# Kernel optimization log

Hardware: AMD Instinct MI355X
Metric: run time of the kernel (lower is better)

The kernel has to match this reference:

```python
import jax, jax.numpy as jnp
import numpy as np

P_X, P_Y = 2, 2  # pooling window (matches init_kwargs)


def setup_inputs() -> dict:
    key = jax.random.key(0)
    k1, k2 = jax.random.split(key)
    B, C, n, m = 32, 64, 128, 128
    s = jax.random.normal(k1, (B, C, n, m), dtype=jnp.float32)
    # multinomial weight vectors, one per (i, j, k) in loop order i->j->k
    etas = jax.random.uniform(k2, (n * m * C, P_X * P_Y), dtype=jnp.float32)
    return {"s": s, "etas": etas}


def reference(s, etas):
    B, C, n, m = s.shape
    P = P_X * P_Y
    # torch.multinomial(eta, 1) == categorical with logits log(eta)
    key = jax.random.key(42)
    logits = jnp.log(jnp.maximum(etas, 1e-30))
    zeta = jax.random.categorical(key, logits, axis=-1)          # [n*m*C]
    # cnt order is (i, j, k) -> reshape to [n, m, C], move C first
    onehot = jax.nn.one_hot(zeta, P, dtype=s.dtype)
    onehot = onehot.reshape(n, m, C, P).transpose(2, 0, 1, 3)     # [C, n, m, P]
    # scatter s value into the sampled slot of each p_x*p_y tile
    tiles = s[..., None] * onehot[None]                           # [B, C, n, m, P]
    tiles = tiles.reshape(B, C, n, m, P_X, P_Y)
    out = tiles.transpose(0, 1, 2, 4, 3, 5).reshape(B, C, n * P_X, m * P_Y)
    return out
```

## Files before the change

### kernel.cpp

```cpp
#include <hip/hip_runtime.h>
#include <math.h>
#include <stdint.h>


#define NROWS 1048576u

#define KS0 0u
#define KS1 42u
#define KS2 0x1BD11BF0u

__device__ __forceinline__ void threefry2x32(uint32_t x0, uint32_t x1,
                                             uint32_t& o0, uint32_t& o1) {
  x0 += KS0; x1 += KS1;
#define TF_RND(R) { x0 += x1; x1 = (x1 << (R)) | (x1 >> (32 - (R))); x1 ^= x0; }
  TF_RND(13) TF_RND(15) TF_RND(26) TF_RND(6)
  x0 += KS1; x1 += KS2 + 1u;
  TF_RND(17) TF_RND(29) TF_RND(16) TF_RND(24)
  x0 += KS2; x1 += KS0 + 2u;
  TF_RND(13) TF_RND(15) TF_RND(26) TF_RND(6)
  x0 += KS0; x1 += KS1 + 3u;
  TF_RND(17) TF_RND(29) TF_RND(16) TF_RND(24)
  x0 += KS1; x1 += KS2 + 4u;
  TF_RND(13) TF_RND(15) TF_RND(26) TF_RND(6)
  x0 += KS2; x1 += KS0 + 5u;
#undef TF_RND
  o0 = x0; o1 = x1;
}

__device__ __forceinline__ float bits_to_unit(uint32_t b) {
  float u = __uint_as_float((b >> 9) | 0x3F800000u) - 1.0f;
  return (u == 0.0f) ? 1.17549435e-38f : u;
}

__device__ __forceinline__ int argmax_gumbel(const float* u, const float* eta) {
  float best = -3.4e38f; int bi = 0;
  #pragma unroll
  for (int p = 0; p < 4; ++p) {
    float inner = (float)log((double)u[p]);
    float g     = -(float)log(-(double)inner);
    float logit = (float)log((double)fmaxf(eta[p], 1e-30f));
    float score = g + logit;
    if (score > best) { best = score; bi = p; }
  }
  return bi;
}

__global__ __launch_bounds__(256) void zeta_kernel(const float4* __restrict__ etas,
                                                   uint8_t* __restrict__ zc) {
  const uint32_t t = blockIdx.x * 256u + threadIdx.x;
  float u[4];
  #pragma unroll
  for (int p = 0; p < 4; ++p) {
    uint32_t o0, o1;
    threefry2x32(0u, 4u * t + (uint32_t)p, o0, o1);
    u[p] = bits_to_unit(o0 ^ o1);
  }
  const float4 e4 = etas[t];
  const float eta[4] = {e4.x, e4.y, e4.z, e4.w};
  const int z = argmax_gumbel(u, eta);
  zc[(t & 63u) * 16384u + (t >> 6)] = (uint8_t)z;
}

__global__ __launch_bounds__(256) void scatter_kernel(const float* __restrict__ s,
                                                      const uint8_t* __restrict__ zc,
                                                      float4* __restrict__ out) {
  const uint32_t t  = blockIdx.x * 256u + threadIdx.x;
  const uint32_t yq = t & 63u;
  const uint32_t x  = (t >> 6) & 255u;
  const uint32_t bc = t >> 14;
  const uint32_t c  = bc & 63u;
  const uint32_t i  = x >> 1, px = x & 1u;
  const uint32_t j0 = yq << 1;
  const float2 s2 = *reinterpret_cast<const float2*>(
      &s[((size_t)bc << 14) + (i << 7) + j0]);
  const uint32_t zidx = c * 16384u + (i << 7) + j0;
  const uint8_t z0 = zc[zidx], z1 = zc[zidx + 1u];
  const uint32_t p0 = px << 1, p1 = p0 + 1u;
  float4 o;
  o.x = (z0 == (uint8_t)p0) ? s2.x : 0.0f;
  o.y = (z0 == (uint8_t)p1) ? s2.x : 0.0f;
  o.z = (z1 == (uint8_t)p0) ? s2.y : 0.0f;
  o.w = (z1 == (uint8_t)p1) ? s2.y : 0.0f;
  out[t] = o;
}

extern "C" void kernel_launch(void* const* d_in, const int* in_sizes, int n_in,
                              void* d_out, int out_size, void* d_ws, size_t ws_size,
                              hipStream_t stream) {
  const float*  s    = (const float*)d_in[0];
  const float4* etas = (const float4*)d_in[1];
  float4*  out = (float4*)d_out;
  uint8_t* zc  = (uint8_t*)d_ws;

  zeta_kernel<<<NROWS / 256u, 256, 0, stream>>>(etas, zc);
  scatter_kernel<<<33554432u / 256u, 256, 0, stream>>>(s, zc, out);
}
```

Before: 653.8 us.

## Use custom double log polynomial and write both pooled rows per thread with nontemporal stores

Replaces libm double-precision log calls in the Gumbel sampling with an inline range-reduced series log, aiming to cut the cost of the zeta kernel. The scatter kernel now has each thread produce both output rows of a 2x2 tile, halving thread count and the redundant reads of s and zeta. Output writes use nontemporal stores so the write stream does not pollute the cache. The custom log may differ from libm in the last bits, which could flip argmax ties and change which slot is sampled.

```diff
diff --git a/kernel.cpp b/kernel.cpp
--- a/kernel.cpp
+++ b/kernel.cpp
@@ -8,6 +8,8 @@
 #define KS0 0u
 #define KS1 42u
 #define KS2 0x1BD11BF0u
+
+typedef float f32x4 __attribute__((ext_vector_type(4)));
 
 __device__ __forceinline__ void threefry2x32(uint32_t x0, uint32_t x1,
                                              uint32_t& o0, uint32_t& o1) {
@@ -32,13 +34,30 @@
   return (u == 0.0f) ? 1.17549435e-38f : u;
 }
 
+__device__ __forceinline__ float log_cr(double x) {
+  const int64_t ib = (int64_t)__double_as_longlong(x);
+  int e = (int)((ib >> 52) & 0x7FF) - 1023;
+  double r = __longlong_as_double((ib & 0xFFFFFFFFFFFFFLL) | 0x3FF0000000000000LL);
+  if (r > 1.4142135623730951) { r *= 0.5; e += 1; }
+  const double s  = (r - 1.0) / (r + 1.0);
+  const double s2 = s * s;
+  double p = fma(s2, 1.0/15.0, 1.0/13.0);
+  p = fma(s2, p, 1.0/11.0);
+  p = fma(s2, p, 1.0/9.0);
+  p = fma(s2, p, 1.0/7.0);
+  p = fma(s2, p, 1.0/5.0);
+  p = fma(s2, p, 1.0/3.0);
+  const double logr = 2.0 * fma(s * s2, p, s);
+  return (float)fma((double)e, 0.6931471805599453, logr);
+}
+
 __device__ __forceinline__ int argmax_gumbel(const float* u, const float* eta) {
   float best = -3.4e38f; int bi = 0;
   #pragma unroll
   for (int p = 0; p < 4; ++p) {
-    float inner = (float)log((double)u[p]);
-    float g     = -(float)log(-(double)inner);
-    float logit = (float)log((double)fmaxf(eta[p], 1e-30f));
+    float inner = log_cr((double)u[p]);
+    float g     = -log_cr(-(double)inner);
+    float logit = log_cr((double)fmaxf(eta[p], 1e-30f));
     float score = g + logit;
     if (score > best) { best = score; bi = p; }
   }
@@ -63,25 +82,29 @@
 
 __global__ __launch_bounds__(256) void scatter_kernel(const float* __restrict__ s,
                                                       const uint8_t* __restrict__ zc,
-                                                      float4* __restrict__ out) {
+                                                      f32x4* __restrict__ out) {
   const uint32_t t  = blockIdx.x * 256u + threadIdx.x;
   const uint32_t yq = t & 63u;
-  const uint32_t x  = (t >> 6) & 255u;
-  const uint32_t bc = t >> 14;
+  const uint32_t i  = (t >> 6) & 127u;
+  const uint32_t bc = t >> 13;
   const uint32_t c  = bc & 63u;
-  const uint32_t i  = x >> 1, px = x & 1u;
   const uint32_t j0 = yq << 1;
   const float2 s2 = *reinterpret_cast<const float2*>(
       &s[((size_t)bc << 14) + (i << 7) + j0]);
   const uint32_t zidx = c * 16384u + (i << 7) + j0;
   const uint8_t z0 = zc[zidx], z1 = zc[zidx + 1u];
-  const uint32_t p0 = px << 1, p1 = p0 + 1u;
-  float4 o;
-  o.x = (z0 == (uint8_t)p0) ? s2.x : 0.0f;
-  o.y = (z0 == (uint8_t)p1) ? s2.x : 0.0f;
-  o.z = (z1 == (uint8_t)p0) ? s2.y : 0.0f;
-  o.w = (z1 == (uint8_t)p1) ? s2.y : 0.0f;
-  out[t] = o;
+  f32x4 o0, o1;
+  o0.x = (z0 == 0) ? s2.x : 0.0f;
+  o0.y = (z0 == 1) ? s2.x : 0.0f;
+  o0.z = (z1 == 0) ? s2.y : 0.0f;
+  o0.w = (z1 == 1) ? s2.y : 0.0f;
+  o1.x = (z0 == 2) ? s2.x : 0.0f;
+  o1.y = (z0 == 3) ? s2.x : 0.0f;
+  o1.z = (z1 == 2) ? s2.y : 0.0f;
+  o1.w = (z1 == 3) ? s2.y : 0.0f;
+  const uint32_t ob = (bc << 14) | (i << 7) | yq;
+  __builtin_nontemporal_store(o0, &out[ob]);
+  __builtin_nontemporal_store(o1, &out[ob + 64u]);
 }
 
 extern "C" void kernel_launch(void* const* d_in, const int* in_sizes, int n_in,
@@ -89,9 +112,9 @@
                               hipStream_t stream) {
   const float*  s    = (const float*)d_in[0];
   const float4* etas = (const float4*)d_in[1];
-  float4*  out = (float4*)d_out;
+  f32x4*   out = (f32x4*)d_out;
   uint8_t* zc  = (uint8_t*)d_ws;
 
   zeta_kernel<<<NROWS / 256u, 256, 0, stream>>>(etas, zc);
-  scatter_kernel<<<33554432u / 256u, 256, 0, stream>>>(s, zc, out);
+  scatter_kernel<<<16777216u / 256u, 256, 0, stream>>>(s, zc, out);
 }
```

After: 630.4 us (median of 2 runs). 3.6% less time.
